# Optimization experiments

Hardware: AMD Instinct MI355X
Metric: run time of the kernel (lower is better)

Reference implementation:

```python
import jax, jax.numpy as jnp
import numpy as np

B, S, H = 4, 1024, 1024
NH, HD = 16, 64            # heads, head_dim (H = NH*HD)
E, K, I = 8, 2, 2048       # experts, top_k, moe_intermediate_size
CAP_FACTOR = 2.0
EPS_RMS = 1e-6
EPS_LN = 1e-6
SCALE = HD ** -0.5


def setup_inputs() -> dict:
    key = jax.random.key(0)
    ks = jax.random.split(key, 12)
    std = 0.02
    causal = jnp.where(jnp.tril(jnp.ones((S, S), bool)), 0.0, -1e9).astype(jnp.float32)
    return {
        "hidden_states": jax.random.normal(ks[0], (B, S, H), jnp.float32),
        "attn_mask": causal[None, None],                       # [1,1,S,S] additive
        "qw": jax.random.normal(ks[1], (H, H), jnp.float32) * std,
        "qb": jnp.zeros((H,), jnp.float32),
        "kw": jax.random.normal(ks[2], (H, H), jnp.float32) * std,
        "kb": jnp.zeros((H,), jnp.float32),
        "vw": jax.random.normal(ks[3], (H, H), jnp.float32) * std,
        "vb": jnp.zeros((H,), jnp.float32),
        "ow": jax.random.normal(ks[4], (H, H), jnp.float32) * std,
        "ob": jnp.zeros((H,), jnp.float32),
        "rms_w": jnp.ones((H,), jnp.float32),
        "gate_w": jax.random.normal(ks[5], (E, H), jnp.float32) * std,
        "w1": jax.random.normal(ks[6], (E, H, I), jnp.float32) * std,
        "b1": jnp.zeros((E, I), jnp.float32),
        "w2": jax.random.normal(ks[7], (E, I, H), jnp.float32) * std,
        "b2": jnp.zeros((E, H), jnp.float32),
        "ln_w": jnp.ones((H,), jnp.float32),
        "ln_b": jnp.zeros((H,), jnp.float32),
    }


def _rmsnorm(x, w):
    v = jnp.mean(x * x, axis=-1, keepdims=True)
    return w * (x * jax.lax.rsqrt(v + EPS_RMS))


def _layernorm(x, w, b):
    mu = jnp.mean(x, axis=-1, keepdims=True)
    var = jnp.mean((x - mu) ** 2, axis=-1, keepdims=True)
    return w * (x - mu) * jax.lax.rsqrt(var + EPS_LN) + b


def reference(hidden_states, attn_mask, qw, qb, kw, kb, vw, vb, ow, ob,
              rms_w, gate_w, w1, b1, w2, b2, ln_w, ln_b):
    x = hidden_states                                            # [B,S,H]
    # ---- attention (eval mode: dropout = identity) ----
    def heads(t):  # [B,S,H] -> [B,NH,S,HD]
        return t.reshape(B, S, NH, HD).transpose(0, 2, 1, 3)
    q = heads(x @ qw + qb)
    k = heads(x @ kw + kb)
    v = heads(x @ vw + vb)
    scores = jnp.einsum("bhqd,bhkd->bhqk", q, k) * SCALE + attn_mask
    p = jax.nn.softmax(scores.astype(jnp.float32), axis=-1).astype(q.dtype)
    ao = jnp.einsum("bhqk,bhkd->bhqd", p, v).transpose(0, 2, 1, 3).reshape(B, S, H)
    ao = ao @ ow + ob
    h = _rmsnorm(x + ao, rms_w)                                  # [B,S,H]
    # ---- MoE ----
    xf = h.reshape(-1, H)                                        # [T,H]
    T = B * S
    router_logits = xf.astype(jnp.float32) @ gate_w.T            # [T,E]
    probs = jax.nn.softmax(router_logits, axis=-1)
    tw, ti = jax.lax.top_k(probs, K)                             # [T,K]
    tw = tw / (jnp.sum(tw, axis=-1, keepdims=True) + 1e-20)      # norm_topk_prob
    tw = tw / K
    # capacity drop (deterministic cumulative-position variant; capacity_factor
    # chosen so no token overflows -> identical to the torch module in eval)
    capacity = int(B * S * K * CAP_FACTOR / E)
    flat = ti.reshape(-1)                                        # [T*K]
    oh = (flat[:, None] == jnp.arange(E)[None, :]).astype(jnp.int32)
    pos = jnp.cumsum(oh, axis=0) - oh                            # slot index per expert
    mypos = jnp.take_along_axis(pos, flat[:, None], axis=1)[:, 0].reshape(T, K)
    tw = jnp.where(mypos >= capacity, 0.0, tw).astype(xf.dtype)
    # dense per-expert FFN + weighted combine
    cw = jnp.sum(jax.nn.one_hot(ti, E, dtype=xf.dtype) * tw[..., None], axis=1)  # [T,E]
    h1 = jax.nn.gelu(jnp.einsum("th,ehi->tei", xf, w1) + b1, approximate=False)
    y = jnp.einsum("tei,eih->teh", h1, w2) + b2                  # [T,E,H]
    routed = jnp.einsum("te,teh->th", cw, y).reshape(B, S, H)
    # ---- final residual + LayerNorm ----
    out = _layernorm(h + routed, ln_w, ln_b)
    return out
```

## Files before the change

kernel.cpp:

```cpp
#include <hip/hip_runtime.h>

#define NB 4
#define SQL 1024
#define HDIM 1024
#define NHEAD 16
#define HEADD 64
#define NEXP 8
#define IDIM 2048
#define NTOK (NB*SQL)
#define CAPACITY 2048
#define ATT_SCALE 0.125f

typedef unsigned short u16;
typedef __attribute__((ext_vector_type(8))) short bf16x8;
typedef __attribute__((ext_vector_type(8))) unsigned short u16x8;
typedef __attribute__((ext_vector_type(4))) float f32x4;

__device__ __forceinline__ u16 f2bf(float f) {
  union { float f; unsigned u; } x; x.f = f;
  unsigned r = (x.u + 0x7fffu + ((x.u >> 16) & 1u)) >> 16;
  return (u16)r;
}
__device__ __forceinline__ float bf2f(u16 b) {
  union { unsigned u; float f; } x; x.u = ((unsigned)b) << 16;
  return x.f;
}
__device__ __forceinline__ float wave_sum(float v) {
#pragma unroll
  for (int off = 32; off > 0; off >>= 1) v += __shfl_xor(v, off);
  return v;
}
__device__ __forceinline__ void gload_lds16(const u16* g, u16* l) {
  __builtin_amdgcn_global_load_lds(
      (const __attribute__((address_space(1))) void*)g,
      (__attribute__((address_space(3))) void*)l, 16, 0, 0);
}

__global__ __launch_bounds__(256)
void cvt_bf16_kernel(const float* __restrict__ in, u16* __restrict__ out)
{
  size_t i = (size_t)blockIdx.x * 1024 + threadIdx.x * 4;
  float4 v = *(const float4*)&in[i];
  ushort4 o = {f2bf(v.x), f2bf(v.y), f2bf(v.z), f2bf(v.w)};
  *(ushort4*)&out[i] = o;
}

__global__ __launch_bounds__(256)
void transpose_cvt_kernel(const float* __restrict__ in, u16* __restrict__ out,
                          int R, int C)
{
  int e = blockIdx.z;
  const float* ine = in + (size_t)e * R * C;
  u16* oute = out + (size_t)e * R * C;
  __shared__ u16 Ts[32 * 34];
  int tx = threadIdx.x & 31, ty = threadIdx.x >> 5;
  int r0 = blockIdx.y * 32, c0 = blockIdx.x * 32;
#pragma unroll
  for (int qq = 0; qq < 4; ++qq) {
    int rr = ty + qq * 8;
    Ts[tx * 34 + rr] = f2bf(ine[(size_t)(r0 + rr) * C + c0 + tx]);
  }
  __syncthreads();
#pragma unroll
  for (int qq = 0; qq < 4; ++qq) {
    int cc = ty + qq * 8;
    oute[(size_t)(c0 + cc) * R + r0 + tx] = Ts[cc * 34 + tx];
  }
}

__global__ __launch_bounds__(256)
void qkv_mfma_kernel(const u16* __restrict__ xbf,
                     const u16* __restrict__ wqT, const u16* __restrict__ wkT,
                     const u16* __restrict__ wvT,
                     const float* __restrict__ bq, const float* __restrict__ bk,
                     const float* __restrict__ bv,
                     u16* __restrict__ q, u16* __restrict__ k, u16* __restrict__ v)
{
  int mode = blockIdx.z;
  const u16* BT   = (mode == 0) ? wqT : (mode == 1) ? wkT : wvT;
  const float* bia = (mode == 0) ? bq : (mode == 1) ? bk : bv;
  u16* dst         = (mode == 0) ? q : (mode == 1) ? k : v;
  int m0 = blockIdx.x * 128, n0 = blockIdx.y * 128;
  __shared__ __align__(16) u16 As[128 * 64];
  __shared__ __align__(16) u16 Bs[128 * 64];
  int tid = threadIdx.x;
  f32x4 acc[4][4];
#pragma unroll
  for (int i = 0; i < 4; ++i)
#pragma unroll
    for (int j = 0; j < 4; ++j) acc[i][j] = (f32x4){0.f, 0.f, 0.f, 0.f};
  int w = tid >> 6, l = tid & 63;
  int lr = l & 15, lq = l >> 4;
  int wm = (w & 1) * 64, wn = (w >> 1) * 64;
  const u16* aptr[4]; const u16* bptr[4]; u16* adst[4]; u16* bdst[4];
#pragma unroll
  for (int p = 0; p < 4; ++p) {
    int flat = p * 256 + tid;
    int r = flat >> 3, c = flat & 7;
    int cs = (c ^ (r & 7)) * 8;
    aptr[p] = xbf + (size_t)(m0 + r) * HDIM + cs;
    bptr[p] = BT + (size_t)(n0 + r) * HDIM + cs;
    adst[p] = &As[(size_t)(p * 256 + w * 64) * 8];
    bdst[p] = &Bs[(size_t)(p * 256 + w * 64) * 8];
  }
  for (int k0 = 0; k0 < HDIM; k0 += 64) {
#pragma unroll
    for (int p = 0; p < 4; ++p) {
      gload_lds16(aptr[p] + k0, adst[p]);
      gload_lds16(bptr[p] + k0, bdst[p]);
    }
    __syncthreads();
#pragma unroll
    for (int s = 0; s < 2; ++s) {
      bf16x8 af[4], bfv[4];
#pragma unroll
      for (int i = 0; i < 4; ++i) {
        int mloc = wm + i * 16 + lr;
        af[i]  = *(const bf16x8*)&As[(mloc * 8 + ((s * 4 + lq) ^ (mloc & 7))) * 8];
        int n = wn + i * 16 + lr;
        bfv[i] = *(const bf16x8*)&Bs[(n * 8 + ((s * 4 + lq) ^ (n & 7))) * 8];
      }
#pragma unroll
      for (int i = 0; i < 4; ++i)
#pragma unroll
        for (int j = 0; j < 4; ++j)
          acc[i][j] = __builtin_amdgcn_mfma_f32_16x16x32_bf16(af[i], bfv[j], acc[i][j], 0, 0, 0);
    }
    __syncthreads();
  }
#pragma unroll
  for (int i = 0; i < 4; ++i)
#pragma unroll
    for (int j = 0; j < 4; ++j) {
      int col = n0 + wn + j * 16 + lr;
      float bb = bia[col];
      int hh = col >> 6, d = col & 63;
#pragma unroll
      for (int r = 0; r < 4; ++r) {
        int tg = m0 + wm + i * 16 + lq * 4 + r;
        int bi = tg >> 10, s = tg & 1023;
        dst[((size_t)(bi * NHEAD + hh) * SQL + s) * HEADD + d] = f2bf(acc[i][j][r] + bb);
      }
    }
}

__global__ __launch_bounds__(256)
void proj_mfma_kernel(const u16* __restrict__ aobf, const u16* __restrict__ owT,
                      const float* __restrict__ ob, float* __restrict__ out)
{
  int m0 = blockIdx.x * 128, n0 = blockIdx.y * 128;
  __shared__ __align__(16) u16 As[128 * 64];
  __shared__ __align__(16) u16 Bs[128 * 64];
  int tid = threadIdx.x;
  f32x4 acc[4][4];
#pragma unroll
  for (int i = 0; i < 4; ++i)
#pragma unroll
    for (int j = 0; j < 4; ++j) acc[i][j] = (f32x4){0.f, 0.f, 0.f, 0.f};
  int w = tid >> 6, l = tid & 63;
  int lr = l & 15, lq = l >> 4;
  int wm = (w & 1) * 64, wn = (w >> 1) * 64;
  const u16* aptr[4]; const u16* bptr[4]; u16* adst[4]; u16* bdst[4];
#pragma unroll
  for (int p = 0; p < 4; ++p) {
    int flat = p * 256 + tid;
    int r = flat >> 3, c = flat & 7;
    int cs = (c ^ (r & 7)) * 8;
    aptr[p] = aobf + (size_t)(m0 + r) * HDIM + cs;
    bptr[p] = owT + (size_t)(n0 + r) * HDIM + cs;
    adst[p] = &As[(size_t)(p * 256 + w * 64) * 8];
    bdst[p] = &Bs[(size_t)(p * 256 + w * 64) * 8];
  }
  for (int k0 = 0; k0 < HDIM; k0 += 64) {
#pragma unroll
    for (int p = 0; p < 4; ++p) {
      gload_lds16(aptr[p] + k0, adst[p]);
      gload_lds16(bptr[p] + k0, bdst[p]);
    }
    __syncthreads();
#pragma unroll
    for (int s = 0; s < 2; ++s) {
      bf16x8 af[4], bfv[4];
#pragma unroll
      for (int i = 0; i < 4; ++i) {
        int mloc = wm + i * 16 + lr;
        af[i]  = *(const bf16x8*)&As[(mloc * 8 + ((s * 4 + lq) ^ (mloc & 7))) * 8];
        int n = wn + i * 16 + lr;
        bfv[i] = *(const bf16x8*)&Bs[(n * 8 + ((s * 4 + lq) ^ (n & 7))) * 8];
      }
#pragma unroll
      for (int i = 0; i < 4; ++i)
#pragma unroll
        for (int j = 0; j < 4; ++j)
          acc[i][j] = __builtin_amdgcn_mfma_f32_16x16x32_bf16(af[i], bfv[j], acc[i][j], 0, 0, 0);
    }
    __syncthreads();
  }
#pragma unroll
  for (int i = 0; i < 4; ++i)
#pragma unroll
    for (int j = 0; j < 4; ++j) {
      int col = n0 + wn + j * 16 + lr;
      float bb = ob[col];
#pragma unroll
      for (int r = 0; r < 4; ++r) {
        int tg = m0 + wm + i * 16 + lq * 4 + r;
        out[(size_t)tg * HDIM + col] = acc[i][j][r] + bb;
      }
    }
}

__global__ __launch_bounds__(256)
void attn_mfma_kernel(const u16* __restrict__ q, const u16* __restrict__ k,
                      const u16* __restrict__ v, u16* __restrict__ ao)
{
  __shared__ __align__(16) u16 VT[64 * 72];
  __shared__ __align__(16) u16 Pl[4][16 * 72];
  int bid = blockIdx.x;
  int bh = bid & 63;
  int qt = 15 - (bid >> 6);
  int q0 = qt * 64;
  int tid = threadIdx.x;
  int w = tid >> 6, l = tid & 63;
  int lr = l & 15, lq = l >> 4;

  const u16* qp = q + ((size_t)bh * SQL + q0 + w * 16 + lr) * HEADD + lq * 8;
  bf16x8 qf0 = *(const bf16x8*)qp;
  bf16x8 qf1 = *(const bf16x8*)(qp + 32);

  float mrow[4], lrow[4];
  f32x4 Ot[4];
#pragma unroll
  for (int r = 0; r < 4; ++r) { mrow[r] = -1e30f; lrow[r] = 0.f; }
#pragma unroll
  for (int j = 0; j < 4; ++j) Ot[j] = (f32x4){0.f, 0.f, 0.f, 0.f};

  int vkey = 2 * (l & 31);
  int vd0 = w * 16 + (l >> 5) * 8;

  for (int kb = 0; kb <= q0; kb += 64) {
    __syncthreads();
    {
      const u16* vp = v + ((size_t)bh * SQL + kb + vkey) * HEADD + vd0;
      u16x8 a = *(const u16x8*)vp;
      u16x8 b = *(const u16x8*)(vp + HEADD);
#pragma unroll
      for (int e = 0; e < 8; ++e) {
        ushort2 pr = {a[e], b[e]};
        *(ushort2*)&VT[(vd0 + e) * 72 + vkey] = pr;
      }
    }
    f32x4 sacc[4];
#pragma unroll
    for (int j = 0; j < 4; ++j) sacc[j] = (f32x4){0.f, 0.f, 0.f, 0.f};
    const u16* kp = k + ((size_t)bh * SQL + kb + lr) * HEADD + lq * 8;
#pragma unroll
    for (int j = 0; j < 4; ++j) {
      bf16x8 kf0 = *(const bf16x8*)(kp + (size_t)j * 16 * HEADD);
      bf16x8 kf1 = *(const bf16x8*)(kp + (size_t)j * 16 * HEADD + 32);
      sacc[j] = __builtin_amdgcn_mfma_f32_16x16x32_bf16(qf0, kf0, sacc[j], 0, 0, 0);
      sacc[j] = __builtin_amdgcn_mfma_f32_16x16x32_bf16(qf1, kf1, sacc[j], 0, 0, 0);
    }
    bool diag = (kb == q0);
    float pv[4][4];
#pragma unroll
    for (int r = 0; r < 4; ++r) {
      float sv[4];
      float rm = -1e30f;
#pragma unroll
      for (int j = 0; j < 4; ++j) {
        float s0 = sacc[j][r] * ATT_SCALE;
        if (diag && (j * 16 + lr) > (w * 16 + lq * 4 + r)) s0 = -1e30f;
        sv[j] = s0;
        rm = fmaxf(rm, s0);
      }
      rm = fmaxf(rm, __shfl_xor(rm, 1));
      rm = fmaxf(rm, __shfl_xor(rm, 2));
      rm = fmaxf(rm, __shfl_xor(rm, 4));
      rm = fmaxf(rm, __shfl_xor(rm, 8));
      float mnew = fmaxf(mrow[r], rm);
      float alpha = __expf(mrow[r] - mnew);
      mrow[r] = mnew;
      float rl = 0.f;
#pragma unroll
      for (int j = 0; j < 4; ++j) {
        float p = __expf(sv[j] - mnew);
        pv[j][r] = p;
        rl += p;
      }
      rl += __shfl_xor(rl, 1);
      rl += __shfl_xor(rl, 2);
      rl += __shfl_xor(rl, 4);
      rl += __shfl_xor(rl, 8);
      lrow[r] = lrow[r] * alpha + rl;
#pragma unroll
      for (int j2 = 0; j2 < 4; ++j2) Ot[j2][r] *= alpha;
    }
#pragma unroll
    for (int j = 0; j < 4; ++j)
#pragma unroll
      for (int r = 0; r < 4; ++r)
        Pl[w][(lq * 4 + r) * 72 + j * 16 + lr] = f2bf(pv[j][r]);
    __syncthreads();
    const u16* pbase = &Pl[w][lr * 72];
#pragma unroll
    for (int s = 0; s < 2; ++s) {
      bf16x8 pa = *(const bf16x8*)(pbase + s * 32 + lq * 8);
#pragma unroll
      for (int j2 = 0; j2 < 4; ++j2) {
        bf16x8 vb = *(const bf16x8*)&VT[(j2 * 16 + lr) * 72 + s * 32 + lq * 8];
        Ot[j2] = __builtin_amdgcn_mfma_f32_16x16x32_bf16(pa, vb, Ot[j2], 0, 0, 0);
      }
    }
  }
  int b = bh >> 4, hh = bh & 15;
#pragma unroll
  for (int r = 0; r < 4; ++r) {
    float invl = 1.0f / lrow[r];
    int row = q0 + w * 16 + lq * 4 + r;
#pragma unroll
    for (int j2 = 0; j2 < 4; ++j2)
      ao[((size_t)(b * SQL + row)) * HDIM + hh * HEADD + j2 * 16 + lr] =
          f2bf(Ot[j2][r] * invl);
  }
}

__global__ __launch_bounds__(256)
void rmsnorm_kernel(const float* __restrict__ x, const float* __restrict__ p,
                    const float* __restrict__ w, float* __restrict__ out,
                    u16* __restrict__ outbf)
{
  int t = blockIdx.x, tid = threadIdx.x;
  float4 xv = ((const float4*)(x + (size_t)t * HDIM))[tid];
  float4 pv = ((const float4*)(p + (size_t)t * HDIM))[tid];
  float4 s = {xv.x + pv.x, xv.y + pv.y, xv.z + pv.z, xv.w + pv.w};
  float ss = s.x * s.x + s.y * s.y + s.z * s.z + s.w * s.w;
  __shared__ float red[4];
  float wsv = wave_sum(ss);
  int wid = tid >> 6, l = tid & 63;
  if (l == 0) red[wid] = wsv;
  __syncthreads();
  float tot = red[0] + red[1] + red[2] + red[3];
  float inv = 1.0f / sqrtf(tot / (float)HDIM + 1e-6f);
  float4 wv = ((const float4*)w)[tid];
  float4 o = {s.x * inv * wv.x, s.y * inv * wv.y, s.z * inv * wv.z, s.w * inv * wv.w};
  ((float4*)(out + (size_t)t * HDIM))[tid] = o;
  ushort4 ob = {f2bf(o.x), f2bf(o.y), f2bf(o.z), f2bf(o.w)};
  ((ushort4*)(outbf + (size_t)t * HDIM))[tid] = ob;
}

__global__ __launch_bounds__(256)
void router_kernel(const float* __restrict__ h, const float* __restrict__ gw,
                   int* __restrict__ ti, float* __restrict__ tw)
{
  int wid = threadIdx.x >> 6, l = threadIdx.x & 63;
  int t = blockIdx.x * 4 + wid;
  const float* hr = h + (size_t)t * HDIM;
  float hv[16];
#pragma unroll
  for (int j = 0; j < 16; ++j) hv[j] = hr[l + 64 * j];
  float lg[NEXP];
#pragma unroll
  for (int e = 0; e < NEXP; ++e) {
    const float* g = gw + (size_t)e * HDIM;
    float p = 0.f;
#pragma unroll
    for (int j = 0; j < 16; ++j) p += hv[j] * g[l + 64 * j];
    lg[e] = wave_sum(p);
  }
  if (l == 0) {
    int i1 = 0; float m1 = lg[0];
#pragma unroll
    for (int e = 1; e < NEXP; ++e) if (lg[e] > m1) { m1 = lg[e]; i1 = e; }
    int i2 = 0; float m2 = -1e30f;
#pragma unroll
    for (int e = 0; e < NEXP; ++e) if (e != i1 && lg[e] > m2) { m2 = lg[e]; i2 = e; }
    float se = 0.f;
#pragma unroll
    for (int e = 0; e < NEXP; ++e) se += expf(lg[e] - m1);
    float p1 = 1.0f / se;
    float p2 = expf(m2 - m1) / se;
    float denom = p1 + p2 + 1e-20f;
    tw[t * 2]     = p1 / denom * 0.5f;
    tw[t * 2 + 1] = p2 / denom * 0.5f;
    ti[t * 2]     = i1;
    ti[t * 2 + 1] = i2;
  }
}

__global__ __launch_bounds__(1024)
void scan_kernel(const int* __restrict__ ti, int* __restrict__ eidx,
                 int* __restrict__ counts, int* __restrict__ slotmap,
                 int* __restrict__ ebase)
{
  __shared__ int wc[16][NEXP];
  __shared__ int wbase[16][NEXP];
  __shared__ int tot[NEXP];
  __shared__ int eb[NEXP];
  int tid = threadIdx.x;
  int w = tid >> 6, l = tid & 63;
  unsigned long long below = (l == 0) ? 0ull : ((~0ull) >> (64 - l));
  const int CH = (NTOK * 2) / 16;
  const int RND = CH / 64;
  int ev[RND];
  int myc[NEXP];
#pragma unroll
  for (int e = 0; e < NEXP; ++e) myc[e] = 0;
#pragma unroll
  for (int c2 = 0; c2 < RND; ++c2) {
    int f = w * CH + c2 * 64 + l;
    int e = ti[f];
    ev[c2] = e;
#pragma unroll
    for (int e0 = 0; e0 < NEXP; ++e0)
      myc[e0] += __popcll(__ballot(e == e0));
  }
  if (l == 0) {
#pragma unroll
    for (int e = 0; e < NEXP; ++e) wc[w][e] = myc[e];
  }
  __syncthreads();
  if (tid < NEXP) {
    int run = 0;
#pragma unroll
    for (int ww = 0; ww < 16; ++ww) { wbase[ww][tid] = run; run += wc[ww][tid]; }
    tot[tid] = run;
    counts[tid] = (run < CAPACITY) ? run : CAPACITY;
  }
  __syncthreads();
  if (tid == 0) {
    int run = 0;
#pragma unroll
    for (int e = 0; e < NEXP; ++e) {
      eb[e] = run;
      ebase[e] = run;
      int c = tot[e];
      run += (c < CAPACITY) ? c : CAPACITY;
    }
  }
  __syncthreads();
  int base[NEXP];
#pragma unroll
  for (int e = 0; e < NEXP; ++e) base[e] = wbase[w][e];
#pragma unroll
  for (int c2 = 0; c2 < RND; ++c2) {
    int f = w * CH + c2 * 64 + l;
    int e = ev[c2];
    int mypos = 0;
#pragma unroll
    for (int e0 = 0; e0 < NEXP; ++e0) {
      unsigned long long mm = __ballot(e == e0);
      if (e == e0) mypos = base[e0] + __popcll(mm & below);
      base[e0] += __popcll(mm);
    }
    int sm_;
    if (mypos < CAPACITY) {
      eidx[e * CAPACITY + mypos] = f >> 1;
      sm_ = eb[e] + mypos;
    } else sm_ = -1;
    slotmap[f] = sm_;
  }
}

__global__ __launch_bounds__(256)
void moe_gemm1_kernel(const u16* __restrict__ hbf, const u16* __restrict__ w1T,
                      const float* __restrict__ b1, const int* __restrict__ eidx,
                      const int* __restrict__ counts, const int* __restrict__ ebase,
                      u16* __restrict__ h1)
{
  int bid = blockIdx.x;
  int e = bid & 7;
  int idx = bid >> 3;
  int m0 = (idx & 15) * 128;
  int n0 = (idx >> 4) * 128;
  int cnt = counts[e];
  if (m0 >= cnt) return;
  int base = ebase[e];
  __shared__ __align__(16) u16 As[128 * 64];
  __shared__ __align__(16) u16 Bs[128 * 64];
  __shared__ int rowtok[128];
  int tid = threadIdx.x;
  if (tid < 128) {
    int r = m0 + tid;
    rowtok[tid] = (r < cnt) ? eidx[e * CAPACITY + r] : 0;
  }
  __syncthreads();
  const u16* BT = w1T + (size_t)e * IDIM * HDIM;
  f32x4 acc[4][4];
#pragma unroll
  for (int i = 0; i < 4; ++i)
#pragma unroll
    for (int j = 0; j < 4; ++j) acc[i][j] = (f32x4){0.f, 0.f, 0.f, 0.f};
  int w = tid >> 6, l = tid & 63;
  int lr = l & 15, lq = l >> 4;
  int wm = (w & 1) * 64, wn = (w >> 1) * 64;
  const u16* aptr[4]; const u16* bptr[4]; u16* adst[4]; u16* bdst[4];
#pragma unroll
  for (int p = 0; p < 4; ++p) {
    int flat = p * 256 + tid;
    int r = flat >> 3, c = flat & 7;
    int cs = (c ^ (r & 7)) * 8;
    aptr[p] = hbf + (size_t)rowtok[r] * HDIM + cs;
    bptr[p] = BT + (size_t)(n0 + r) * HDIM + cs;
    adst[p] = &As[(size_t)(p * 256 + w * 64) * 8];
    bdst[p] = &Bs[(size_t)(p * 256 + w * 64) * 8];
  }
  for (int k0 = 0; k0 < HDIM; k0 += 64) {
#pragma unroll
    for (int p = 0; p < 4; ++p) {
      gload_lds16(aptr[p] + k0, adst[p]);
      gload_lds16(bptr[p] + k0, bdst[p]);
    }
    __syncthreads();
#pragma unroll
    for (int s = 0; s < 2; ++s) {
      bf16x8 af[4], bfv[4];
#pragma unroll
      for (int i = 0; i < 4; ++i) {
        int mloc = wm + i * 16 + lr;
        af[i]  = *(const bf16x8*)&As[(mloc * 8 + ((s * 4 + lq) ^ (mloc & 7))) * 8];
        int n = wn + i * 16 + lr;
        bfv[i] = *(const bf16x8*)&Bs[(n * 8 + ((s * 4 + lq) ^ (n & 7))) * 8];
      }
#pragma unroll
      for (int i = 0; i < 4; ++i)
#pragma unroll
        for (int j = 0; j < 4; ++j)
          acc[i][j] = __builtin_amdgcn_mfma_f32_16x16x32_bf16(af[i], bfv[j], acc[i][j], 0, 0, 0);
    }
    __syncthreads();
  }
#pragma unroll
  for (int i = 0; i < 4; ++i)
#pragma unroll
    for (int j = 0; j < 4; ++j) {
      int col = n0 + wn + j * 16 + lr;
      float bb = b1[(size_t)e * IDIM + col];
#pragma unroll
      for (int r = 0; r < 4; ++r) {
        int rowl = m0 + wm + i * 16 + lq * 4 + r;
        if (rowl < cnt) {
          float y = acc[i][j][r] + bb;
          float g = 0.5f * y * (1.0f + erff(y * 0.70710678118654752f));
          h1[(size_t)(base + rowl) * IDIM + col] = f2bf(g);
        }
      }
    }
}

__global__ __launch_bounds__(256)
void moe_gemm2_kernel(const u16* __restrict__ h1, const u16* __restrict__ w2T,
                      const float* __restrict__ b2, const int* __restrict__ counts,
                      const int* __restrict__ ebase, u16* __restrict__ ybuf)
{
  int bid = blockIdx.x;
  int e = bid & 7;
  int idx = bid >> 3;
  int m0 = (idx & 15) * 128;
  int n0 = (idx >> 4) * 128;
  int cnt = counts[e];
  if (m0 >= cnt) return;
  int base = ebase[e];
  __shared__ __align__(16) u16 As[128 * 64];
  __shared__ __align__(16) u16 Bs[128 * 64];
  int tid = threadIdx.x;
  const u16* BT = w2T + (size_t)e * HDIM * IDIM;
  f32x4 acc[4][4];
#pragma unroll
  for (int i = 0; i < 4; ++i)
#pragma unroll
    for (int j = 0; j < 4; ++j) acc[i][j] = (f32x4){0.f, 0.f, 0.f, 0.f};
  int w = tid >> 6, l = tid & 63;
  int lr = l & 15, lq = l >> 4;
  int wm = (w & 1) * 64, wn = (w >> 1) * 64;
  const u16* aptr[4]; const u16* bptr[4]; u16* adst[4]; u16* bdst[4];
#pragma unroll
  for (int p = 0; p < 4; ++p) {
    int flat = p * 256 + tid;
    int r = flat >> 3, c = flat & 7;
    int cs = (c ^ (r & 7)) * 8;
    int rowg = m0 + r;
    if (rowg >= cnt) rowg = cnt - 1;
    aptr[p] = h1 + (size_t)(base + rowg) * IDIM + cs;
    bptr[p] = BT + (size_t)(n0 + r) * IDIM + cs;
    adst[p] = &As[(size_t)(p * 256 + w * 64) * 8];
    bdst[p] = &Bs[(size_t)(p * 256 + w * 64) * 8];
  }
  for (int k0 = 0; k0 < IDIM; k0 += 64) {
#pragma unroll
    for (int p = 0; p < 4; ++p) {
      gload_lds16(aptr[p] + k0, adst[p]);
      gload_lds16(bptr[p] + k0, bdst[p]);
    }
    __syncthreads();
#pragma unroll
    for (int s = 0; s < 2; ++s) {
      bf16x8 af[4], bfv[4];
#pragma unroll
      for (int i = 0; i < 4; ++i) {
        int mloc = wm + i * 16 + lr;
        af[i]  = *(const bf16x8*)&As[(mloc * 8 + ((s * 4 + lq) ^ (mloc & 7))) * 8];
        int n = wn + i * 16 + lr;
        bfv[i] = *(const bf16x8*)&Bs[(n * 8 + ((s * 4 + lq) ^ (n & 7))) * 8];
      }
#pragma unroll
      for (int i = 0; i < 4; ++i)
#pragma unroll
        for (int j = 0; j < 4; ++j)
          acc[i][j] = __builtin_amdgcn_mfma_f32_16x16x32_bf16(af[i], bfv[j], acc[i][j], 0, 0, 0);
    }
    __syncthreads();
  }
#pragma unroll
  for (int i = 0; i < 4; ++i)
#pragma unroll
    for (int j = 0; j < 4; ++j) {
      int col = n0 + wn + j * 16 + lr;
      float bb = b2[(size_t)e * HDIM + col];
#pragma unroll
      for (int r = 0; r < 4; ++r) {
        int rowl = m0 + wm + i * 16 + lq * 4 + r;
        if (rowl < cnt)
          ybuf[(size_t)(base + rowl) * HDIM + col] = f2bf(acc[i][j][r] + bb);
      }
    }
}

__global__ __launch_bounds__(256)
void final_kernel(const float* __restrict__ h, const u16* __restrict__ ybuf,
                  const int* __restrict__ slotmap, const float* __restrict__ tw,
                  const float* __restrict__ lnw, const float* __restrict__ lnb,
                  float* __restrict__ out)
{
  int t = blockIdx.x, tid = threadIdx.x;
  int s0 = slotmap[t * 2], s1 = slotmap[t * 2 + 1];
  float w0 = tw[t * 2], w1v = tw[t * 2 + 1];
  float4 hv = ((const float4*)(h + (size_t)t * HDIM))[tid];
  float vals[4] = {hv.x, hv.y, hv.z, hv.w};
  if (s0 >= 0) {
    const u16* yr = ybuf + (size_t)s0 * HDIM + tid * 4;
#pragma unroll
    for (int j = 0; j < 4; ++j) vals[j] += w0 * bf2f(yr[j]);
  }
  if (s1 >= 0) {
    const u16* yr = ybuf + (size_t)s1 * HDIM + tid * 4;
#pragma unroll
    for (int j = 0; j < 4; ++j) vals[j] += w1v * bf2f(yr[j]);
  }
  float s = vals[0] + vals[1] + vals[2] + vals[3];
  float q2 = vals[0] * vals[0] + vals[1] * vals[1] + vals[2] * vals[2] + vals[3] * vals[3];
  __shared__ float reds[4], redq[4];
  float wsv = wave_sum(s), wqv = wave_sum(q2);
  int wid = tid >> 6, l = tid & 63;
  if (l == 0) { reds[wid] = wsv; redq[wid] = wqv; }
  __syncthreads();
  float tot = reds[0] + reds[1] + reds[2] + reds[3];
  float totq = redq[0] + redq[1] + redq[2] + redq[3];
  float mu = tot / 1024.0f;
  float var = totq / 1024.0f - mu * mu;
  float inv = 1.0f / sqrtf(var + 1e-6f);
#pragma unroll
  for (int j = 0; j < 4; ++j) {
    int c = tid * 4 + j;
    out[(size_t)t * HDIM + c] = (vals[j] - mu) * inv * lnw[c] + lnb[c];
  }
}

extern "C" void kernel_launch(void* const* d_in, const int* in_sizes, int n_in,
                              void* d_out, int out_size, void* d_ws, size_t ws_size,
                              hipStream_t stream)
{
  const float* x      = (const float*)d_in[0];
  const float* qw     = (const float*)d_in[2];
  const float* qb     = (const float*)d_in[3];
  const float* kw     = (const float*)d_in[4];
  const float* kb     = (const float*)d_in[5];
  const float* vw     = (const float*)d_in[6];
  const float* vb     = (const float*)d_in[7];
  const float* ow     = (const float*)d_in[8];
  const float* ob     = (const float*)d_in[9];
  const float* rms_w  = (const float*)d_in[10];
  const float* gate_w = (const float*)d_in[11];
  const float* w1     = (const float*)d_in[12];
  const float* b1     = (const float*)d_in[13];
  const float* w2     = (const float*)d_in[14];
  const float* b2     = (const float*)d_in[15];
  const float* ln_w   = (const float*)d_in[16];
  const float* ln_b   = (const float*)d_in[17];

  char* ws = (char*)d_ws;
  const size_t MB = 1024ull * 1024ull;
  u16*   qbf    = (u16*)(ws + 0 * MB);
  u16*   kbf    = (u16*)(ws + 8 * MB);
  u16*   vbf    = (u16*)(ws + 16 * MB);
  u16*   aobf   = (u16*)(ws + 24 * MB);
  u16*   xbf    = (u16*)(ws + 32 * MB);
  u16*   wqT    = (u16*)(ws + 40 * MB);
  u16*   wkT    = (u16*)(ws + 42 * MB);
  u16*   wvT    = (u16*)(ws + 44 * MB);
  u16*   owT    = (u16*)(ws + 46 * MB);
  float* projbuf= (float*)(ws + 48 * MB);
  float* hbuf   = (float*)(ws + 64 * MB);
  u16*   hbf    = (u16*)(ws + 80 * MB);
  u16*   wT     = (u16*)(ws + 0 * MB);
  u16*   ybuf   = (u16*)(ws + 32 * MB);
  u16*   h1buf  = (u16*)(ws + 88 * MB);
  char*  sm     = ws + 120 * MB;
  int*   ti      = (int*)(sm);
  float* tw      = (float*)(sm + 32 * 1024);
  int*   eidx    = (int*)(sm + 64 * 1024);
  int*   slotmap = (int*)(sm + 128 * 1024);
  int*   counts  = (int*)(sm + 160 * 1024);
  int*   ebase   = (int*)(sm + 164 * 1024);

  cvt_bf16_kernel<<<NTOK, 256, 0, stream>>>(x, xbf);
  transpose_cvt_kernel<<<dim3(32, 32, 1), 256, 0, stream>>>(qw, wqT, HDIM, HDIM);
  transpose_cvt_kernel<<<dim3(32, 32, 1), 256, 0, stream>>>(kw, wkT, HDIM, HDIM);
  transpose_cvt_kernel<<<dim3(32, 32, 1), 256, 0, stream>>>(vw, wvT, HDIM, HDIM);
  transpose_cvt_kernel<<<dim3(32, 32, 1), 256, 0, stream>>>(ow, owT, HDIM, HDIM);
  qkv_mfma_kernel<<<dim3(NTOK / 128, HDIM / 128, 3), 256, 0, stream>>>(
      xbf, wqT, wkT, wvT, qb, kb, vb, qbf, kbf, vbf);
  attn_mfma_kernel<<<NB * NHEAD * (SQL / 64), 256, 0, stream>>>(qbf, kbf, vbf, aobf);
  proj_mfma_kernel<<<dim3(NTOK / 128, HDIM / 128), 256, 0, stream>>>(
      aobf, owT, ob, projbuf);
  rmsnorm_kernel<<<NTOK, 256, 0, stream>>>(x, projbuf, rms_w, hbuf, hbf);
  transpose_cvt_kernel<<<dim3(IDIM / 32, HDIM / 32, NEXP), 256, 0, stream>>>(
      w1, wT, HDIM, IDIM);
  router_kernel<<<NTOK / 4, 256, 0, stream>>>(hbuf, gate_w, ti, tw);
  scan_kernel<<<1, 1024, 0, stream>>>(ti, eidx, counts, slotmap, ebase);
  moe_gemm1_kernel<<<dim3(NEXP * (CAPACITY / 128) * (IDIM / 128)), 256, 0, stream>>>(
      hbf, wT, b1, eidx, counts, ebase, h1buf);
  transpose_cvt_kernel<<<dim3(HDIM / 32, IDIM / 32, NEXP), 256, 0, stream>>>(
      w2, wT, IDIM, HDIM);
  moe_gemm2_kernel<<<dim3(NEXP * (CAPACITY / 128) * (HDIM / 128)), 256, 0, stream>>>(
      h1buf, wT, b2, counts, ebase, ybuf);
  final_kernel<<<NTOK, 256, 0, stream>>>(hbuf, ybuf, slotmap, tw, ln_w, ln_b,
                                         (float*)d_out);
}
```

Measured before the change: 534.1 us.

## Double-buffer LDS tiles in all MFMA GEMM kernels to overlap loads

```diff
diff --git a/kernel.cpp b/kernel.cpp
--- a/kernel.cpp
+++ b/kernel.cpp
@@ -68,6 +68,7 @@
   }
 }
 
+
 __global__ __launch_bounds__(256)
 void qkv_mfma_kernel(const u16* __restrict__ xbf,
                      const u16* __restrict__ wqT, const u16* __restrict__ wkT,
@@ -81,8 +82,8 @@
   const float* bia = (mode == 0) ? bq : (mode == 1) ? bk : bv;
   u16* dst         = (mode == 0) ? q : (mode == 1) ? k : v;
   int m0 = blockIdx.x * 128, n0 = blockIdx.y * 128;
-  __shared__ __align__(16) u16 As[128 * 64];
-  __shared__ __align__(16) u16 Bs[128 * 64];
+  __shared__ __align__(16) u16 As[2 * 128 * 64];
+  __shared__ __align__(16) u16 Bs[2 * 128 * 64];
   int tid = threadIdx.x;
   f32x4 acc[4][4];
 #pragma unroll
@@ -103,22 +104,33 @@
     adst[p] = &As[(size_t)(p * 256 + w * 64) * 8];
     bdst[p] = &Bs[(size_t)(p * 256 + w * 64) * 8];
   }
-  for (int k0 = 0; k0 < HDIM; k0 += 64) {
-#pragma unroll
-    for (int p = 0; p < 4; ++p) {
-      gload_lds16(aptr[p] + k0, adst[p]);
-      gload_lds16(bptr[p] + k0, bdst[p]);
-    }
+#pragma unroll
+  for (int p = 0; p < 4; ++p) { gload_lds16(aptr[p], adst[p]); gload_lds16(bptr[p], bdst[p]); }
+  const int NT = HDIM / 64;
+#pragma unroll
+  for (int t = 0; t < NT; ++t) {
+    const int cur = t & 1;
     __syncthreads();
+    if (t + 1 < NT) {
+      int k0 = (t + 1) * 64;
+      int off = (cur ^ 1) * (128 * 64);
+#pragma unroll
+      for (int p = 0; p < 4; ++p) {
+        gload_lds16(aptr[p] + k0, adst[p] + off);
+        gload_lds16(bptr[p] + k0, bdst[p] + off);
+      }
+    }
+    const u16* Ab = As + cur * (128 * 64);
+    const u16* Bb = Bs + cur * (128 * 64);
 #pragma unroll
     for (int s = 0; s < 2; ++s) {
       bf16x8 af[4], bfv[4];
 #pragma unroll
       for (int i = 0; i < 4; ++i) {
         int mloc = wm + i * 16 + lr;
-        af[i]  = *(const bf16x8*)&As[(mloc * 8 + ((s * 4 + lq) ^ (mloc & 7))) * 8];
+        af[i]  = *(const bf16x8*)&Ab[(mloc * 8 + ((s * 4 + lq) ^ (mloc & 7))) * 8];
         int n = wn + i * 16 + lr;
-        bfv[i] = *(const bf16x8*)&Bs[(n * 8 + ((s * 4 + lq) ^ (n & 7))) * 8];
+        bfv[i] = *(const bf16x8*)&Bb[(n * 8 + ((s * 4 + lq) ^ (n & 7))) * 8];
       }
 #pragma unroll
       for (int i = 0; i < 4; ++i)
@@ -126,7 +138,6 @@
         for (int j = 0; j < 4; ++j)
           acc[i][j] = __builtin_amdgcn_mfma_f32_16x16x32_bf16(af[i], bfv[j], acc[i][j], 0, 0, 0);
     }
-    __syncthreads();
   }
 #pragma unroll
   for (int i = 0; i < 4; ++i)
@@ -149,8 +160,8 @@
                       const float* __restrict__ ob, float* __restrict__ out)
 {
   int m0 = blockIdx.x * 128, n0 = blockIdx.y * 128;
-  __shared__ __align__(16) u16 As[128 * 64];
-  __shared__ __align__(16) u16 Bs[128 * 64];
+  __shared__ __align__(16) u16 As[2 * 128 * 64];
+  __shared__ __align__(16) u16 Bs[2 * 128 * 64];
   int tid = threadIdx.x;
   f32x4 acc[4][4];
 #pragma unroll
@@ -171,22 +182,33 @@
     adst[p] = &As[(size_t)(p * 256 + w * 64) * 8];
     bdst[p] = &Bs[(size_t)(p * 256 + w * 64) * 8];
   }
-  for (int k0 = 0; k0 < HDIM; k0 += 64) {
-#pragma unroll
-    for (int p = 0; p < 4; ++p) {
-      gload_lds16(aptr[p] + k0, adst[p]);
-      gload_lds16(bptr[p] + k0, bdst[p]);
-    }
+#pragma unroll
+  for (int p = 0; p < 4; ++p) { gload_lds16(aptr[p], adst[p]); gload_lds16(bptr[p], bdst[p]); }
+  const int NT = HDIM / 64;
+#pragma unroll
+  for (int t = 0; t < NT; ++t) {
+    const int cur = t & 1;
     __syncthreads();
+    if (t + 1 < NT) {
+      int k0 = (t + 1) * 64;
+      int off = (cur ^ 1) * (128 * 64);
+#pragma unroll
+      for (int p = 0; p < 4; ++p) {
+        gload_lds16(aptr[p] + k0, adst[p] + off);
+        gload_lds16(bptr[p] + k0, bdst[p] + off);
+      }
+    }
+    const u16* Ab = As + cur * (128 * 64);
+    const u16* Bb = Bs + cur * (128 * 64);
 #pragma unroll
     for (int s = 0; s < 2; ++s) {
       bf16x8 af[4], bfv[4];
 #pragma unroll
       for (int i = 0; i < 4; ++i) {
         int mloc = wm + i * 16 + lr;
-        af[i]  = *(const bf16x8*)&As[(mloc * 8 + ((s * 4 + lq) ^ (mloc & 7))) * 8];
+        af[i]  = *(const bf16x8*)&Ab[(mloc * 8 + ((s * 4 + lq) ^ (mloc & 7))) * 8];
         int n = wn + i * 16 + lr;
-        bfv[i] = *(const bf16x8*)&Bs[(n * 8 + ((s * 4 + lq) ^ (n & 7))) * 8];
+        bfv[i] = *(const bf16x8*)&Bb[(n * 8 + ((s * 4 + lq) ^ (n & 7))) * 8];
       }
 #pragma unroll
       for (int i = 0; i < 4; ++i)
@@ -194,7 +216,6 @@
         for (int j = 0; j < 4; ++j)
           acc[i][j] = __builtin_amdgcn_mfma_f32_16x16x32_bf16(af[i], bfv[j], acc[i][j], 0, 0, 0);
     }
-    __syncthreads();
   }
 #pragma unroll
   for (int i = 0; i < 4; ++i)
@@ -476,8 +497,8 @@
   int cnt = counts[e];
   if (m0 >= cnt) return;
   int base = ebase[e];
-  __shared__ __align__(16) u16 As[128 * 64];
-  __shared__ __align__(16) u16 Bs[128 * 64];
+  __shared__ __align__(16) u16 As[2 * 128 * 64];
+  __shared__ __align__(16) u16 Bs[2 * 128 * 64];
   __shared__ int rowtok[128];
   int tid = threadIdx.x;
   if (tid < 128) {
@@ -505,22 +526,33 @@
     adst[p] = &As[(size_t)(p * 256 + w * 64) * 8];
     bdst[p] = &Bs[(size_t)(p * 256 + w * 64) * 8];
   }
-  for (int k0 = 0; k0 < HDIM; k0 += 64) {
-#pragma unroll
-    for (int p = 0; p < 4; ++p) {
-      gload_lds16(aptr[p] + k0, adst[p]);
-      gload_lds16(bptr[p] + k0, bdst[p]);
-    }
+#pragma unroll
+  for (int p = 0; p < 4; ++p) { gload_lds16(aptr[p], adst[p]); gload_lds16(bptr[p], bdst[p]); }
+  const int NT = HDIM / 64;
+#pragma unroll
+  for (int t = 0; t < NT; ++t) {
+    const int cur = t & 1;
     __syncthreads();
+    if (t + 1 < NT) {
+      int k0 = (t + 1) * 64;
+      int off = (cur ^ 1) * (128 * 64);
+#pragma unroll
+      for (int p = 0; p < 4; ++p) {
+        gload_lds16(aptr[p] + k0, adst[p] + off);
+        gload_lds16(bptr[p] + k0, bdst[p] + off);
+      }
+    }
+    const u16* Ab = As + cur * (128 * 64);
+    const u16* Bb = Bs + cur * (128 * 64);
 #pragma unroll
     for (int s = 0; s < 2; ++s) {
       bf16x8 af[4], bfv[4];
 #pragma unroll
       for (int i = 0; i < 4; ++i) {
         int mloc = wm + i * 16 + lr;
-        af[i]  = *(const bf16x8*)&As[(mloc * 8 + ((s * 4 + lq) ^ (mloc & 7))) * 8];
+        af[i]  = *(const bf16x8*)&Ab[(mloc * 8 + ((s * 4 + lq) ^ (mloc & 7))) * 8];
         int n = wn + i * 16 + lr;
-        bfv[i] = *(const bf16x8*)&Bs[(n * 8 + ((s * 4 + lq) ^ (n & 7))) * 8];
+        bfv[i] = *(const bf16x8*)&Bb[(n * 8 + ((s * 4 + lq) ^ (n & 7))) * 8];
       }
 #pragma unroll
       for (int i = 0; i < 4; ++i)
@@ -528,7 +560,6 @@
         for (int j = 0; j < 4; ++j)
           acc[i][j] = __builtin_amdgcn_mfma_f32_16x16x32_bf16(af[i], bfv[j], acc[i][j], 0, 0, 0);
     }
-    __syncthreads();
   }
 #pragma unroll
   for (int i = 0; i < 4; ++i)
@@ -561,8 +592,8 @@
   int cnt = counts[e];
   if (m0 >= cnt) return;
   int base = ebase[e];
-  __shared__ __align__(16) u16 As[128 * 64];
-  __shared__ __align__(16) u16 Bs[128 * 64];
+  __shared__ __align__(16) u16 As[2 * 128 * 64];
+  __shared__ __align__(16) u16 Bs[2 * 128 * 64];
   int tid = threadIdx.x;
   const u16* BT = w2T + (size_t)e * HDIM * IDIM;
   f32x4 acc[4][4];
@@ -586,22 +617,33 @@
     adst[p] = &As[(size_t)(p * 256 + w * 64) * 8];
     bdst[p] = &Bs[(size_t)(p * 256 + w * 64) * 8];
   }
-  for (int k0 = 0; k0 < IDIM; k0 += 64) {
-#pragma unroll
-    for (int p = 0; p < 4; ++p) {
-      gload_lds16(aptr[p] + k0, adst[p]);
-      gload_lds16(bptr[p] + k0, bdst[p]);
-    }
+#pragma unroll
+  for (int p = 0; p < 4; ++p) { gload_lds16(aptr[p], adst[p]); gload_lds16(bptr[p], bdst[p]); }
+  const int NT = IDIM / 64;
+#pragma unroll
+  for (int t = 0; t < NT; ++t) {
+    const int cur = t & 1;
     __syncthreads();
+    if (t + 1 < NT) {
+      int k0 = (t + 1) * 64;
+      int off = (cur ^ 1) * (128 * 64);
+#pragma unroll
+      for (int p = 0; p < 4; ++p) {
+        gload_lds16(aptr[p] + k0, adst[p] + off);
+        gload_lds16(bptr[p] + k0, bdst[p] + off);
+      }
+    }
+    const u16* Ab = As + cur * (128 * 64);
+    const u16* Bb = Bs + cur * (128 * 64);
 #pragma unroll
     for (int s = 0; s < 2; ++s) {
       bf16x8 af[4], bfv[4];
 #pragma unroll
       for (int i = 0; i < 4; ++i) {
         int mloc = wm + i * 16 + lr;
-        af[i]  = *(const bf16x8*)&As[(mloc * 8 + ((s * 4 + lq) ^ (mloc & 7))) * 8];
+        af[i]  = *(const bf16x8*)&Ab[(mloc * 8 + ((s * 4 + lq) ^ (mloc & 7))) * 8];
         int n = wn + i * 16 + lr;
-        bfv[i] = *(const bf16x8*)&Bs[(n * 8 + ((s * 4 + lq) ^ (n & 7))) * 8];
+        bfv[i] = *(const bf16x8*)&Bb[(n * 8 + ((s * 4 + lq) ^ (n & 7))) * 8];
       }
 #pragma unroll
       for (int i = 0; i < 4; ++i)
@@ -609,7 +651,6 @@
         for (int j = 0; j < 4; ++j)
           acc[i][j] = __builtin_amdgcn_mfma_f32_16x16x32_bf16(af[i], bfv[j], acc[i][j], 0, 0, 0);
     }
-    __syncthreads();
   }
 #pragma unroll
   for (int i = 0; i < 4; ++i)
```

New measurement: 526.7 us. About the same (-1.4%).

## Double-buffer LDS tiles in GEMM kernels and hoist w2 transpose

Applied to the files above, without the earlier changes.

```diff
diff --git a/kernel.cpp b/kernel.cpp
--- a/kernel.cpp
+++ b/kernel.cpp
@@ -81,8 +81,10 @@
   const float* bia = (mode == 0) ? bq : (mode == 1) ? bk : bv;
   u16* dst         = (mode == 0) ? q : (mode == 1) ? k : v;
   int m0 = blockIdx.x * 128, n0 = blockIdx.y * 128;
-  __shared__ __align__(16) u16 As[128 * 64];
-  __shared__ __align__(16) u16 Bs[128 * 64];
+  __shared__ __align__(16) u16 As0[128 * 64];
+  __shared__ __align__(16) u16 As1[128 * 64];
+  __shared__ __align__(16) u16 Bs0[128 * 64];
+  __shared__ __align__(16) u16 Bs1[128 * 64];
   int tid = threadIdx.x;
   f32x4 acc[4][4];
 #pragma unroll
@@ -92,7 +94,7 @@
   int w = tid >> 6, l = tid & 63;
   int lr = l & 15, lq = l >> 4;
   int wm = (w & 1) * 64, wn = (w >> 1) * 64;
-  const u16* aptr[4]; const u16* bptr[4]; u16* adst[4]; u16* bdst[4];
+  const u16* aptr[4]; const u16* bptr[4];
 #pragma unroll
   for (int p = 0; p < 4; ++p) {
     int flat = p * 256 + tid;
@@ -100,25 +102,25 @@
     int cs = (c ^ (r & 7)) * 8;
     aptr[p] = xbf + (size_t)(m0 + r) * HDIM + cs;
     bptr[p] = BT + (size_t)(n0 + r) * HDIM + cs;
-    adst[p] = &As[(size_t)(p * 256 + w * 64) * 8];
-    bdst[p] = &Bs[(size_t)(p * 256 + w * 64) * 8];
-  }
-  for (int k0 = 0; k0 < HDIM; k0 += 64) {
+  }
+  auto STAGE = [&](u16* A, u16* B, int k0) {
 #pragma unroll
     for (int p = 0; p < 4; ++p) {
-      gload_lds16(aptr[p] + k0, adst[p]);
-      gload_lds16(bptr[p] + k0, bdst[p]);
-    }
-    __syncthreads();
+      size_t o = (size_t)(p * 256 + w * 64) * 8;
+      gload_lds16(aptr[p] + k0, A + o);
+      gload_lds16(bptr[p] + k0, B + o);
+    }
+  };
+  auto COMPUTE = [&](const u16* Ab, const u16* Bb) {
 #pragma unroll
     for (int s = 0; s < 2; ++s) {
       bf16x8 af[4], bfv[4];
 #pragma unroll
       for (int i = 0; i < 4; ++i) {
         int mloc = wm + i * 16 + lr;
-        af[i]  = *(const bf16x8*)&As[(mloc * 8 + ((s * 4 + lq) ^ (mloc & 7))) * 8];
+        af[i]  = *(const bf16x8*)&Ab[(mloc * 8 + ((s * 4 + lq) ^ (mloc & 7))) * 8];
         int n = wn + i * 16 + lr;
-        bfv[i] = *(const bf16x8*)&Bs[(n * 8 + ((s * 4 + lq) ^ (n & 7))) * 8];
+        bfv[i] = *(const bf16x8*)&Bb[(n * 8 + ((s * 4 + lq) ^ (n & 7))) * 8];
       }
 #pragma unroll
       for (int i = 0; i < 4; ++i)
@@ -126,7 +128,16 @@
         for (int j = 0; j < 4; ++j)
           acc[i][j] = __builtin_amdgcn_mfma_f32_16x16x32_bf16(af[i], bfv[j], acc[i][j], 0, 0, 0);
     }
+  };
+  const int NT = HDIM / 64;
+  STAGE(As0, Bs0, 0);
+  for (int t = 0; t < NT; t += 2) {
     __syncthreads();
+    if (t + 1 < NT) STAGE(As1, Bs1, (t + 1) * 64);
+    COMPUTE(As0, Bs0);
+    __syncthreads();
+    if (t + 2 < NT) STAGE(As0, Bs0, (t + 2) * 64);
+    COMPUTE(As1, Bs1);
   }
 #pragma unroll
   for (int i = 0; i < 4; ++i)
@@ -149,8 +160,10 @@
                       const float* __restrict__ ob, float* __restrict__ out)
 {
   int m0 = blockIdx.x * 128, n0 = blockIdx.y * 128;
-  __shared__ __align__(16) u16 As[128 * 64];
-  __shared__ __align__(16) u16 Bs[128 * 64];
+  __shared__ __align__(16) u16 As0[128 * 64];
+  __shared__ __align__(16) u16 As1[128 * 64];
+  __shared__ __align__(16) u16 Bs0[128 * 64];
+  __shared__ __align__(16) u16 Bs1[128 * 64];
   int tid = threadIdx.x;
   f32x4 acc[4][4];
 #pragma unroll
@@ -160,7 +173,7 @@
   int w = tid >> 6, l = tid & 63;
   int lr = l & 15, lq = l >> 4;
   int wm = (w & 1) * 64, wn = (w >> 1) * 64;
-  const u16* aptr[4]; const u16* bptr[4]; u16* adst[4]; u16* bdst[4];
+  const u16* aptr[4]; const u16* bptr[4];
 #pragma unroll
   for (int p = 0; p < 4; ++p) {
     int flat = p * 256 + tid;
@@ -168,25 +181,25 @@
     int cs = (c ^ (r & 7)) * 8;
     aptr[p] = aobf + (size_t)(m0 + r) * HDIM + cs;
     bptr[p] = owT + (size_t)(n0 + r) * HDIM + cs;
-    adst[p] = &As[(size_t)(p * 256 + w * 64) * 8];
-    bdst[p] = &Bs[(size_t)(p * 256 + w * 64) * 8];
-  }
-  for (int k0 = 0; k0 < HDIM; k0 += 64) {
+  }
+  auto STAGE = [&](u16* A, u16* B, int k0) {
 #pragma unroll
     for (int p = 0; p < 4; ++p) {
-      gload_lds16(aptr[p] + k0, adst[p]);
-      gload_lds16(bptr[p] + k0, bdst[p]);
-    }
-    __syncthreads();
+      size_t o = (size_t)(p * 256 + w * 64) * 8;
+      gload_lds16(aptr[p] + k0, A + o);
+      gload_lds16(bptr[p] + k0, B + o);
+    }
+  };
+  auto COMPUTE = [&](const u16* Ab, const u16* Bb) {
 #pragma unroll
     for (int s = 0; s < 2; ++s) {
       bf16x8 af[4], bfv[4];
 #pragma unroll
       for (int i = 0; i < 4; ++i) {
         int mloc = wm + i * 16 + lr;
-        af[i]  = *(const bf16x8*)&As[(mloc * 8 + ((s * 4 + lq) ^ (mloc & 7))) * 8];
+        af[i]  = *(const bf16x8*)&Ab[(mloc * 8 + ((s * 4 + lq) ^ (mloc & 7))) * 8];
         int n = wn + i * 16 + lr;
-        bfv[i] = *(const bf16x8*)&Bs[(n * 8 + ((s * 4 + lq) ^ (n & 7))) * 8];
+        bfv[i] = *(const bf16x8*)&Bb[(n * 8 + ((s * 4 + lq) ^ (n & 7))) * 8];
       }
 #pragma unroll
       for (int i = 0; i < 4; ++i)
@@ -194,7 +207,16 @@
         for (int j = 0; j < 4; ++j)
           acc[i][j] = __builtin_amdgcn_mfma_f32_16x16x32_bf16(af[i], bfv[j], acc[i][j], 0, 0, 0);
     }
+  };
+  const int NT = HDIM / 64;
+  STAGE(As0, Bs0, 0);
+  for (int t = 0; t < NT; t += 2) {
     __syncthreads();
+    if (t + 1 < NT) STAGE(As1, Bs1, (t + 1) * 64);
+    COMPUTE(As0, Bs0);
+    __syncthreads();
+    if (t + 2 < NT) STAGE(As0, Bs0, (t + 2) * 64);
+    COMPUTE(As1, Bs1);
   }
 #pragma unroll
   for (int i = 0; i < 4; ++i)
@@ -476,8 +498,10 @@
   int cnt = counts[e];
   if (m0 >= cnt) return;
   int base = ebase[e];
-  __shared__ __align__(16) u16 As[128 * 64];
-  __shared__ __align__(16) u16 Bs[128 * 64];
+  __shared__ __align__(16) u16 As0[128 * 64];
+  __shared__ __align__(16) u16 As1[128 * 64];
+  __shared__ __align__(16) u16 Bs0[128 * 64];
+  __shared__ __align__(16) u16 Bs1[128 * 64];
   __shared__ int rowtok[128];
   int tid = threadIdx.x;
   if (tid < 128) {
@@ -494,7 +518,7 @@
   int w = tid >> 6, l = tid & 63;
   int lr = l & 15, lq = l >> 4;
   int wm = (w & 1) * 64, wn = (w >> 1) * 64;
-  const u16* aptr[4]; const u16* bptr[4]; u16* adst[4]; u16* bdst[4];
+  const u16* aptr[4]; const u16* bptr[4];
 #pragma unroll
   for (int p = 0; p < 4; ++p) {
     int flat = p * 256 + tid;
@@ -502,25 +526,25 @@
     int cs = (c ^ (r & 7)) * 8;
     aptr[p] = hbf + (size_t)rowtok[r] * HDIM + cs;
     bptr[p] = BT + (size_t)(n0 + r) * HDIM + cs;
-    adst[p] = &As[(size_t)(p * 256 + w * 64) * 8];
-    bdst[p] = &Bs[(size_t)(p * 256 + w * 64) * 8];
-  }
-  for (int k0 = 0; k0 < HDIM; k0 += 64) {
+  }
+  auto STAGE = [&](u16* A, u16* B, int k0) {
 #pragma unroll
     for (int p = 0; p < 4; ++p) {
-      gload_lds16(aptr[p] + k0, adst[p]);
-      gload_lds16(bptr[p] + k0, bdst[p]);
-    }
-    __syncthreads();
+      size_t o = (size_t)(p * 256 + w * 64) * 8;
+      gload_lds16(aptr[p] + k0, A + o);
+      gload_lds16(bptr[p] + k0, B + o);
+    }
+  };
+  auto COMPUTE = [&](const u16* Ab, const u16* Bb) {
 #pragma unroll
     for (int s = 0; s < 2; ++s) {
       bf16x8 af[4], bfv[4];
 #pragma unroll
       for (int i = 0; i < 4; ++i) {
         int mloc = wm + i * 16 + lr;
-        af[i]  = *(const bf16x8*)&As[(mloc * 8 + ((s * 4 + lq) ^ (mloc & 7))) * 8];
+        af[i]  = *(const bf16x8*)&Ab[(mloc * 8 + ((s * 4 + lq) ^ (mloc & 7))) * 8];
         int n = wn + i * 16 + lr;
-        bfv[i] = *(const bf16x8*)&Bs[(n * 8 + ((s * 4 + lq) ^ (n & 7))) * 8];
+        bfv[i] = *(const bf16x8*)&Bb[(n * 8 + ((s * 4 + lq) ^ (n & 7))) * 8];
       }
 #pragma unroll
       for (int i = 0; i < 4; ++i)
@@ -528,7 +552,35 @@
         for (int j = 0; j < 4; ++j)
           acc[i][j] = __builtin_amdgcn_mfma_f32_16x16x32_bf16(af[i], bfv[j], acc[i][j], 0, 0, 0);
     }
-    __syncthreads();
+  };
+  const int NT = HDIM / 64;
+  STAGE(As0, Bs0, 0);
+#pragma unroll 1
+  for (int t = 0; t < NT; t += 2) {
+    __builtin_amdgcn_s_barrier();
+    __builtin_amdgcn_sched_barrier(0);
+    if (t + 1 < NT) {
+      STAGE(As1, Bs1, (t + 1) * 64);
+      asm volatile("s_waitcnt vmcnt(8)" ::: "memory");
+    } else {
+      asm volatile("s_waitcnt vmcnt(0)" ::: "memory");
+    }
+    __builtin_amdgcn_sched_barrier(0);
+    __builtin_amdgcn_s_barrier();
+    __builtin_amdgcn_sched_barrier(0);
+    COMPUTE(As0, Bs0);
+    __builtin_amdgcn_s_barrier();
+    __builtin_amdgcn_sched_barrier(0);
+    if (t + 2 < NT) {
+      STAGE(As0, Bs0, (t + 2) * 64);
+      asm volatile("s_waitcnt vmcnt(8)" ::: "memory");
+    } else {
+      asm volatile("s_waitcnt vmcnt(0)" ::: "memory");
+    }
+    __builtin_amdgcn_sched_barrier(0);
+    __builtin_amdgcn_s_barrier();
+    __builtin_amdgcn_sched_barrier(0);
+    COMPUTE(As1, Bs1);
   }
 #pragma unroll
   for (int i = 0; i < 4; ++i)
@@ -561,8 +613,10 @@
   int cnt = counts[e];
   if (m0 >= cnt) return;
   int base = ebase[e];
-  __shared__ __align__(16) u16 As[128 * 64];
-  __shared__ __align__(16) u16 Bs[128 * 64];
+  __shared__ __align__(16) u16 As0[128 * 64];
+  __shared__ __align__(16) u16 As1[128 * 64];
+  __shared__ __align__(16) u16 Bs0[128 * 64];
+  __shared__ __align__(16) u16 Bs1[128 * 64];
   int tid = threadIdx.x;
   const u16* BT = w2T + (size_t)e * HDIM * IDIM;
   f32x4 acc[4][4];
@@ -573,7 +627,7 @@
   int w = tid >> 6, l = tid & 63;
   int lr = l & 15, lq = l >> 4;
   int wm = (w & 1) * 64, wn = (w >> 1) * 64;
-  const u16* aptr[4]; const u16* bptr[4]; u16* adst[4]; u16* bdst[4];
+  const u16* aptr[4]; const u16* bptr[4];
 #pragma unroll
   for (int p = 0; p < 4; ++p) {
     int flat = p * 256 + tid;
@@ -583,25 +637,25 @@
     if (rowg >= cnt) rowg = cnt - 1;
     aptr[p] = h1 + (size_t)(base + rowg) * IDIM + cs;
     bptr[p] = BT + (size_t)(n0 + r) * IDIM + cs;
-    adst[p] = &As[(size_t)(p * 256 + w * 64) * 8];
-    bdst[p] = &Bs[(size_t)(p * 256 + w * 64) * 8];
-  }
-  for (int k0 = 0; k0 < IDIM; k0 += 64) {
+  }
+  auto STAGE = [&](u16* A, u16* B, int k0) {
 #pragma unroll
     for (int p = 0; p < 4; ++p) {
-      gload_lds16(aptr[p] + k0, adst[p]);
-      gload_lds16(bptr[p] + k0, bdst[p]);
-    }
-    __syncthreads();
+      size_t o = (size_t)(p * 256 + w * 64) * 8;
+      gload_lds16(aptr[p] + k0, A + o);
+      gload_lds16(bptr[p] + k0, B + o);
+    }
+  };
+  auto COMPUTE = [&](const u16* Ab, const u16* Bb) {
 #pragma unroll
     for (int s = 0; s < 2; ++s) {
       bf16x8 af[4], bfv[4];
 #pragma unroll
       for (int i = 0; i < 4; ++i) {
         int mloc = wm + i * 16 + lr;
-        af[i]  = *(const bf16x8*)&As[(mloc * 8 + ((s * 4 + lq) ^ (mloc & 7))) * 8];
+        af[i]  = *(const bf16x8*)&Ab[(mloc * 8 + ((s * 4 + lq) ^ (mloc & 7))) * 8];
         int n = wn + i * 16 + lr;
-        bfv[i] = *(const bf16x8*)&Bs[(n * 8 + ((s * 4 + lq) ^ (n & 7))) * 8];
+        bfv[i] = *(const bf16x8*)&Bb[(n * 8 + ((s * 4 + lq) ^ (n & 7))) * 8];
       }
 #pragma unroll
       for (int i = 0; i < 4; ++i)
@@ -609,7 +663,35 @@
         for (int j = 0; j < 4; ++j)
           acc[i][j] = __builtin_amdgcn_mfma_f32_16x16x32_bf16(af[i], bfv[j], acc[i][j], 0, 0, 0);
     }
-    __syncthreads();
+  };
+  const int NT = IDIM / 64;
+  STAGE(As0, Bs0, 0);
+#pragma unroll 1
+  for (int t = 0; t < NT; t += 2) {
+    __builtin_amdgcn_s_barrier();
+    __builtin_amdgcn_sched_barrier(0);
+    if (t + 1 < NT) {
+      STAGE(As1, Bs1, (t + 1) * 64);
+      asm volatile("s_waitcnt vmcnt(8)" ::: "memory");
+    } else {
+      asm volatile("s_waitcnt vmcnt(0)" ::: "memory");
+    }
+    __builtin_amdgcn_sched_barrier(0);
+    __builtin_amdgcn_s_barrier();
+    __builtin_amdgcn_sched_barrier(0);
+    COMPUTE(As0, Bs0);
+    __builtin_amdgcn_s_barrier();
+    __builtin_amdgcn_sched_barrier(0);
+    if (t + 2 < NT) {
+      STAGE(As0, Bs0, (t + 2) * 64);
+      asm volatile("s_waitcnt vmcnt(8)" ::: "memory");
+    } else {
+      asm volatile("s_waitcnt vmcnt(0)" ::: "memory");
+    }
+    __builtin_amdgcn_sched_barrier(0);
+    __builtin_amdgcn_s_barrier();
+    __builtin_amdgcn_sched_barrier(0);
+    COMPUTE(As1, Bs1);
   }
 #pragma unroll
   for (int i = 0; i < 4; ++i)
@@ -712,6 +794,8 @@
   int*   slotmap = (int*)(sm + 128 * 1024);
   int*   counts  = (int*)(sm + 160 * 1024);
   int*   ebase   = (int*)(sm + 164 * 1024);
+  bool   sepw2   = ws_size >= 156 * MB;
+  u16*   w2T     = sepw2 ? (u16*)(ws + 124 * MB) : wT;
 
   cvt_bf16_kernel<<<NTOK, 256, 0, stream>>>(x, xbf);
   transpose_cvt_kernel<<<dim3(32, 32, 1), 256, 0, stream>>>(qw, wqT, HDIM, HDIM);
@@ -726,14 +810,18 @@
   rmsnorm_kernel<<<NTOK, 256, 0, stream>>>(x, projbuf, rms_w, hbuf, hbf);
   transpose_cvt_kernel<<<dim3(IDIM / 32, HDIM / 32, NEXP), 256, 0, stream>>>(
       w1, wT, HDIM, IDIM);
+  if (sepw2)
+    transpose_cvt_kernel<<<dim3(HDIM / 32, IDIM / 32, NEXP), 256, 0, stream>>>(
+        w2, w2T, IDIM, HDIM);
   router_kernel<<<NTOK / 4, 256, 0, stream>>>(hbuf, gate_w, ti, tw);
   scan_kernel<<<1, 1024, 0, stream>>>(ti, eidx, counts, slotmap, ebase);
   moe_gemm1_kernel<<<dim3(NEXP * (CAPACITY / 128) * (IDIM / 128)), 256, 0, stream>>>(
       hbf, wT, b1, eidx, counts, ebase, h1buf);
-  transpose_cvt_kernel<<<dim3(HDIM / 32, IDIM / 32, NEXP), 256, 0, stream>>>(
-      w2, wT, IDIM, HDIM);
+  if (!sepw2)
+    transpose_cvt_kernel<<<dim3(HDIM / 32, IDIM / 32, NEXP), 256, 0, stream>>>(
+        w2, w2T, IDIM, HDIM);
   moe_gemm2_kernel<<<dim3(NEXP * (CAPACITY / 128) * (HDIM / 128)), 256, 0, stream>>>(
-      h1buf, wT, b2, counts, ebase, ybuf);
+      h1buf, w2T, b2, counts, ebase, ybuf);
   final_kernel<<<NTOK, 256, 0, stream>>>(hbuf, ybuf, slotmap, tw, ln_w, ln_b,
                                          (float*)d_out);
 }
```

After: 547.0 us. 1.02x slower.
